# Optimization experiments

Hardware: AMD Instinct MI355X
Metric: run time of the kernel (lower is better)

Reference implementation:

```python
import jax, jax.numpy as jnp
import numpy as np

CHANNELS = 128


def setup_inputs() -> dict:
    key = jax.random.key(0)
    ks = jax.random.split(key, 7)
    B, N, C, E = 1, 50000, CHANNELS, 800000
    in_dim = 2 * C + 2  # channels*2 + 2
    tokens = jax.random.normal(ks[0], (B, N, C), dtype=jnp.float32)
    coords = jax.random.normal(ks[1], (B, N, 2), dtype=jnp.float32)
    edge_index = jax.random.randint(ks[2], (2, E), 0, N, dtype=jnp.int64)
    # MLP params: Linear(in_dim, C) -> ReLU -> Linear(C, 1)
    w1 = jax.random.normal(ks[3], (in_dim, C), dtype=jnp.float32) / np.sqrt(in_dim)
    b1 = jnp.zeros((C,), dtype=jnp.float32)
    w2 = jax.random.normal(ks[4], (C, 1), dtype=jnp.float32) / np.sqrt(C)
    b2 = jnp.zeros((1,), dtype=jnp.float32)
    return {"tokens": tokens, "coords": coords, "edge_index": edge_index,
            "w1": w1, "b1": b1, "w2": w2, "b2": b2}


def reference(tokens, coords, edge_index, w1, b1, w2, b2):
    src = edge_index[0]
    dst = edge_index[1]
    x_src = tokens[:, src, :]               # [B, E, C]
    x_dst = tokens[:, dst, :]               # [B, E, C]
    delta = coords[:, dst, :] - coords[:, src, :]  # [B, E, 2]
    feat = jnp.concatenate([x_src, x_dst, delta], axis=-1)  # [B, E, 2C+2]
    h = jax.nn.relu(jnp.einsum('bef,fh->beh', feat, w1) + b1)  # [B, E, C]
    return jnp.einsum('beh,ho->beo', h, w2) + b2               # [B, E, 1]
```

## Files before the change

kernel.cpp:

```cpp
#include <hip/hip_runtime.h>

static constexpr int CH   = 128;
static constexpr int KPAD = 192;

typedef __attribute__((ext_vector_type(8))) short bf16x8;
typedef __attribute__((ext_vector_type(4))) float f32x4;
typedef __attribute__((ext_vector_type(2))) unsigned int u32x2;

__device__ inline unsigned short f2bf(float x) {
    unsigned int u = __float_as_uint(x);
    unsigned int r = (u + 0x7fffu + ((u >> 16) & 1u)) >> 16;
    return (unsigned short)r;
}
__device__ inline unsigned int pack2bf(float a, float b) {
    return (unsigned int)f2bf(a) | ((unsigned int)f2bf(b) << 16);
}

__global__ __launch_bounds__(256) void idx_prep(
    const unsigned int* __restrict__ idxw, uint2* __restrict__ idx2,
    long long E, long long Epad) {
    unsigned nz = 0;
    const int lane = threadIdx.x & 63;
    for (int i = lane; i < 128; i += 64) nz |= idxw[2 * i + 1];
    const int is64 = (__ballot(nz != 0u) == 0ULL) ? 1 : 0;
    const long long stride = (long long)gridDim.x * blockDim.x;
    for (long long i = (long long)blockIdx.x * blockDim.x + threadIdx.x;
         i < Epad; i += stride) {
        uint2 v = make_uint2(0u, 0u);
        if (i < E) {
            const unsigned s = is64 ? idxw[2 * i] : idxw[i];
            const unsigned d = is64 ? idxw[2 * (E + i)] : idxw[E + i];
            v = make_uint2(s << 7, d << 7);
        }
        idx2[i] = v;
    }
}

__global__ __launch_bounds__(256) void w1_prep2(const float* __restrict__ w1,
                                                const float* __restrict__ b1,
                                                unsigned short* __restrict__ Wf) {
    const int gid = blockIdx.x * 256 + threadIdx.x;
    if (gid >= 4 * 5 * 4 * 64) return;
    const int lane = gid & 63;
    const int seg  = gid >> 6;
    const int m    = seg & 3;
    const int ks   = (seg >> 2) % 5;
    const int w    = seg / 20;
    const int c    = w * 64 + m * 16 + (lane & 15);
    const int k0   = ks * 32 + (lane >> 4) * 8;
    const bool isQ = c >= 128;
    const int cc   = c & 127;
    const float sgn = isQ ? 1.f : -1.f;
    unsigned int out[4];
#pragma unroll
    for (int h = 0; h < 4; ++h) {
        float v[2];
#pragma unroll
        for (int j = 0; j < 2; ++j) {
            const int k = k0 + 2 * h + j;
            float x;
            if (k < 128)       x = isQ ? w1[(size_t)(128 + k) * CH + cc]
                                       : w1[(size_t)k * CH + cc];
            else if (k == 128) x = sgn * w1[(size_t)(2 * CH) * CH + cc];
            else if (k == 129) x = sgn * w1[(size_t)(2 * CH + 1) * CH + cc];
            else if (k == 130) x = isQ ? b1[cc] : 0.f;
            else               x = 0.f;
            v[j] = x;
        }
        out[h] = pack2bf(v[0], v[1]);
    }
    *(uint4*)&Wf[(size_t)gid * 8] = make_uint4(out[0], out[1], out[2], out[3]);
}

__global__ __launch_bounds__(256) void node_mfma5(
    const float* __restrict__ tokens, const float* __restrict__ coords,
    const unsigned short* __restrict__ Wf, unsigned short* __restrict__ Plo,
    unsigned short* __restrict__ Phi, unsigned short* __restrict__ Qlo,
    unsigned short* __restrict__ Qhi, int N) {
    __shared__ unsigned short Atile[32 * KPAD];

    const int t    = threadIdx.x;
    const int l    = t & 63;
    const int wid  = t >> 6;
    const int n0   = blockIdx.x * 32;
    const int bl   = l & 15;
    const int bh   = l >> 4;

#pragma unroll
    for (int it = 0; it < 2; ++it) {
        const int idx  = it * 256 + t;
        const int node = idx >> 4;
        const int cq   = idx & 15;
        float4 v0 = make_float4(0.f, 0.f, 0.f, 0.f);
        float4 v1 = v0;
        if (n0 + node < N) {
            const float* src = &tokens[(size_t)(n0 + node) * CH + cq * 8];
            v0 = *(const float4*)src;
            v1 = *(const float4*)(src + 4);
        }
        uint4 u;
        u.x = pack2bf(v0.x, v0.y);
        u.y = pack2bf(v0.z, v0.w);
        u.z = pack2bf(v1.x, v1.y);
        u.w = pack2bf(v1.z, v1.w);
        const int byte = node * 384 + ((cq * 16) ^ ((node & 7) << 4));
        *(uint4*)((char*)Atile + byte) = u;
    }
    {
        const int node = t >> 3;
        const int ce   = t & 7;
        uint4 u = make_uint4(0u, 0u, 0u, 0u);
        if (ce == 0 && n0 + node < N) {
            const float cx = coords[2 * (n0 + node)];
            const float cy = coords[2 * (n0 + node) + 1];
            u.x = pack2bf(cx, cy);
            u.y = pack2bf(1.f, 0.f);
        }
        const int byte = node * 384 + (((16 + ce) * 16) ^ ((node & 7) << 4));
        *(uint4*)((char*)Atile + byte) = u;
    }
    __syncthreads();

    f32x4 acc[4][2];
#pragma unroll
    for (int m = 0; m < 4; ++m)
#pragma unroll
        for (int n = 0; n < 2; ++n) acc[m][n] = (f32x4){0.f, 0.f, 0.f, 0.f};

#pragma unroll
    for (int ks = 0; ks < 5; ++ks) {
        bf16x8 wfrag[4], tfrag[2];
#pragma unroll
        for (int m = 0; m < 4; ++m)
            wfrag[m] = *(const bf16x8*)&Wf[(size_t)(((wid * 5 + ks) * 4 + m) * 64
                                                    + l) * 8];
#pragma unroll
        for (int n = 0; n < 2; ++n) {
            const int row  = n * 16 + bl;
            const int byte = row * 384 + ((ks * 64 + bh * 16) ^ ((row & 7) << 4));
            tfrag[n] = *(const bf16x8*)((const char*)Atile + byte);
        }
#pragma unroll
        for (int m = 0; m < 4; ++m)
#pragma unroll
            for (int n = 0; n < 2; ++n)
                acc[m][n] = __builtin_amdgcn_mfma_f32_16x16x32_bf16(
                    wfrag[m], tfrag[n], acc[m][n], 0, 0, 0);
    }

    unsigned short* dst = (wid == 0) ? Plo : (wid == 1) ? Phi
                          : (wid == 2) ? Qlo : Qhi;
#pragma unroll
    for (int m = 0; m < 4; ++m) {
        const int col = m * 16 + bh * 4;
#pragma unroll
        for (int n = 0; n < 2; ++n) {
            const int node = n0 + n * 16 + bl;
            if (node < N) {
                uint2 val;
                val.x = pack2bf(acc[m][n][0], acc[m][n][1]);
                val.y = pack2bf(acc[m][n][2], acc[m][n][3]);
                *(uint2*)&dst[(size_t)node * 64 + col] = val;
            }
        }
    }
}

template <int PASS>
__global__ __launch_bounds__(256) void edge_pass(
    const unsigned int* __restrict__ idx2w, const unsigned short* __restrict__ Pb,
    const unsigned short* __restrict__ Qb, const float* __restrict__ w2,
    const float* __restrict__ b2, float* __restrict__ partial,
    float* __restrict__ out, long long E) {
    const int t  = threadIdx.x;
    const int gl = t & 7;
    const long long nq = (E + 3) >> 2;
    const long long g0 = (long long)blockIdx.x * 32 + (t >> 3);
    const long long ng = (long long)gridDim.x * 32;
    const float4 wa = *(const float4*)&w2[PASS * 64 + gl * 8];
    const float4 wb = *(const float4*)&w2[PASS * 64 + gl * 8 + 4];
    const float bias = b2[0];
    const char* P = (const char*)Pb;
    const char* Q = (const char*)Qb;

    for (long long q = g0; q < nq; q += ng) {
        const long long e0 = q << 2;
        const u32x2 iv = __builtin_nontemporal_load(
            (const u32x2*)&idx2w[(e0 + (gl & 3)) * 2]);
        unsigned soff[4], doff[4];
#pragma unroll
        for (int j = 0; j < 4; ++j) {
            soff[j] = __shfl(iv.x, j, 8);
            doff[j] = __shfl(iv.y, j, 8);
        }
        uint4 pv[4], qv[4];
#pragma unroll
        for (int j = 0; j < 4; ++j)
            pv[j] = *(const uint4*)(P + soff[j] + 16 * gl);
#pragma unroll
        for (int j = 0; j < 4; ++j)
            qv[j] = *(const uint4*)(Q + doff[j] + 16 * gl);

        float part[4];
#pragma unroll
        for (int j = 0; j < 4; ++j) {
            const float wv[8] = {wa.x, wa.y, wa.z, wa.w, wb.x, wb.y, wb.z, wb.w};
            const unsigned pw[4] = {pv[j].x, pv[j].y, pv[j].z, pv[j].w};
            const unsigned qw[4] = {qv[j].x, qv[j].y, qv[j].z, qv[j].w};
            float acc = 0.f;
#pragma unroll
            for (int i = 0; i < 4; ++i) {
                const float plo = __uint_as_float(pw[i] << 16);
                const float phi = __uint_as_float(pw[i] & 0xffff0000u);
                const float qlo = __uint_as_float(qw[i] << 16);
                const float qhi = __uint_as_float(qw[i] & 0xffff0000u);
                acc = fmaf(fmaxf(plo + qlo, 0.f), wv[2 * i], acc);
                acc = fmaf(fmaxf(phi + qhi, 0.f), wv[2 * i + 1], acc);
            }
            part[j] = acc;
        }

        float t0 = part[0] + __shfl_xor(part[0], 1);
        float t1 = part[1] + __shfl_xor(part[1], 1);
        float t2 = part[2] + __shfl_xor(part[2], 1);
        float t3 = part[3] + __shfl_xor(part[3], 1);
        float a0 = (gl & 1) ? t1 : t0;
        float a1 = (gl & 1) ? t3 : t2;
        a0 += __shfl_xor(a0, 2);
        a1 += __shfl_xor(a1, 2);
        float c = (gl & 2) ? a1 : a0;
        c += __shfl_xor(c, 4);

        const long long e = e0 + gl;
        if (gl < 4 && e < E) {
            if (PASS == 0) {
                __builtin_nontemporal_store(c, &partial[e]);
            } else {
                out[e] = __builtin_nontemporal_load(&partial[e]) + c + bias;
            }
        }
    }
}

extern "C" void kernel_launch(void* const* d_in, const int* in_sizes, int n_in,
                              void* d_out, int out_size, void* d_ws,
                              size_t ws_size, hipStream_t stream) {
    const float* tokens = (const float*)d_in[0];
    const float* coords = (const float*)d_in[1];
    const unsigned int* idxw = (const unsigned int*)d_in[2];
    const float* w1 = (const float*)d_in[3];
    const float* b1 = (const float*)d_in[4];
    const float* w2 = (const float*)d_in[5];
    const float* b2 = (const float*)d_in[6];
    float* out = (float*)d_out;

    const int N = in_sizes[0] / CH;
    const long long E = in_sizes[2] / 2;
    const long long Epad = ((E + 3) >> 2) << 2;

    unsigned short* Plo = (unsigned short*)d_ws;
    unsigned short* Phi = Plo + (size_t)N * 64;
    unsigned short* Qlo = Phi + (size_t)N * 64;
    unsigned short* Qhi = Qlo + (size_t)N * 64;
    uint2* idx2 = (uint2*)(Qhi + (size_t)N * 64);
    unsigned short* Wf = (unsigned short*)(idx2 + Epad);
    float* partial = (float*)(Wf + 5120 * 8);

    idx_prep<<<1024, 256, 0, stream>>>(idxw, idx2, E, Epad);
    w1_prep2<<<20, 256, 0, stream>>>(w1, b1, Wf);

    node_mfma5<<<(N + 31) / 32, 256, 0, stream>>>(tokens, coords, Wf,
                                                  Plo, Phi, Qlo, Qhi, N);

    edge_pass<0><<<4096, 256, 0, stream>>>((const unsigned int*)idx2, Plo, Qlo,
                                           w2, b2, partial, out, E);
    edge_pass<1><<<4096, 256, 0, stream>>>((const unsigned int*)idx2, Phi, Qhi,
                                           w2, b2, partial, out, E);
}
```

Baseline: 77.45 us.

## Split edge gather into four 32-channel passes with quarter-width node tables

Node projection outputs are stored as eight 32-channel bf16 slabs instead of four 64-channel slabs, and the edge stage runs as four passes, each gathering a 64-byte row per endpoint. The aim is to shrink each pass's gathered working set so the random row gathers fit better in cache. The cost is two extra kernel launches, more index reads, and extra read-modify-write traffic on the partial buffer.

```diff
diff --git a/kernel.cpp b/kernel.cpp
--- a/kernel.cpp
+++ b/kernel.cpp
@@ -30,7 +30,7 @@
         if (i < E) {
             const unsigned s = is64 ? idxw[2 * i] : idxw[i];
             const unsigned d = is64 ? idxw[2 * (E + i)] : idxw[E + i];
-            v = make_uint2(s << 7, d << 7);
+            v = make_uint2(s << 6, d << 6);
         }
         idx2[i] = v;
     }
@@ -72,11 +72,10 @@
     *(uint4*)&Wf[(size_t)gid * 8] = make_uint4(out[0], out[1], out[2], out[3]);
 }
 
-__global__ __launch_bounds__(256) void node_mfma5(
+__global__ __launch_bounds__(256) void node_mfma6(
     const float* __restrict__ tokens, const float* __restrict__ coords,
-    const unsigned short* __restrict__ Wf, unsigned short* __restrict__ Plo,
-    unsigned short* __restrict__ Phi, unsigned short* __restrict__ Qlo,
-    unsigned short* __restrict__ Qhi, int N) {
+    const unsigned short* __restrict__ Wf, unsigned short* __restrict__ PQall,
+    int N) {
     __shared__ unsigned short Atile[32 * KPAD];
 
     const int t    = threadIdx.x;
@@ -148,11 +147,12 @@
                     wfrag[m], tfrag[n], acc[m][n], 0, 0, 0);
     }
 
-    unsigned short* dst = (wid == 0) ? Plo : (wid == 1) ? Phi
-                          : (wid == 2) ? Qlo : Qhi;
 #pragma unroll
     for (int m = 0; m < 4; ++m) {
-        const int col = m * 16 + bh * 4;
+        const int c = wid * 64 + m * 16 + bh * 4;
+        const int q = (c < CH) ? (c >> 5) : (4 + ((c & 127) >> 5));
+        unsigned short* dst = PQall + (size_t)q * N * 32;
+        const int col = c & 31;
 #pragma unroll
         for (int n = 0; n < 2; ++n) {
             const int node = n0 + n * 16 + bl;
@@ -160,38 +160,37 @@
                 uint2 val;
                 val.x = pack2bf(acc[m][n][0], acc[m][n][1]);
                 val.y = pack2bf(acc[m][n][2], acc[m][n][3]);
-                *(uint2*)&dst[(size_t)node * 64 + col] = val;
+                *(uint2*)&dst[(size_t)node * 32 + col] = val;
             }
         }
     }
 }
 
 template <int PASS>
-__global__ __launch_bounds__(256) void edge_pass(
-    const unsigned int* __restrict__ idx2w, const unsigned short* __restrict__ Pb,
-    const unsigned short* __restrict__ Qb, const float* __restrict__ w2,
-    const float* __restrict__ b2, float* __restrict__ partial,
-    float* __restrict__ out, long long E) {
+__global__ __launch_bounds__(256) void edge_pass4(
+    const unsigned int* __restrict__ idx2w, const unsigned short* __restrict__ PQall,
+    const float* __restrict__ w2, const float* __restrict__ b2,
+    float* __restrict__ partial, float* __restrict__ out, long long E, int N) {
     const int t  = threadIdx.x;
-    const int gl = t & 7;
+    const int gl = t & 3;
     const long long nq = (E + 3) >> 2;
-    const long long g0 = (long long)blockIdx.x * 32 + (t >> 3);
-    const long long ng = (long long)gridDim.x * 32;
-    const float4 wa = *(const float4*)&w2[PASS * 64 + gl * 8];
-    const float4 wb = *(const float4*)&w2[PASS * 64 + gl * 8 + 4];
+    const long long g0 = (long long)blockIdx.x * 64 + (t >> 2);
+    const long long ng = (long long)gridDim.x * 64;
+    const float4 wa = *(const float4*)&w2[PASS * 32 + gl * 8];
+    const float4 wb = *(const float4*)&w2[PASS * 32 + gl * 8 + 4];
     const float bias = b2[0];
-    const char* P = (const char*)Pb;
-    const char* Q = (const char*)Qb;
+    const char* P = (const char*)(PQall + (size_t)PASS * N * 32);
+    const char* Q = (const char*)(PQall + (size_t)(4 + PASS) * N * 32);
 
     for (long long q = g0; q < nq; q += ng) {
         const long long e0 = q << 2;
         const u32x2 iv = __builtin_nontemporal_load(
-            (const u32x2*)&idx2w[(e0 + (gl & 3)) * 2]);
+            (const u32x2*)&idx2w[(e0 + gl) * 2]);
         unsigned soff[4], doff[4];
 #pragma unroll
         for (int j = 0; j < 4; ++j) {
-            soff[j] = __shfl(iv.x, j, 8);
-            doff[j] = __shfl(iv.y, j, 8);
+            soff[j] = __shfl(iv.x, j, 4);
+            doff[j] = __shfl(iv.y, j, 4);
         }
         uint4 pv[4], qv[4];
 #pragma unroll
@@ -228,13 +227,15 @@
         float a1 = (gl & 1) ? t3 : t2;
         a0 += __shfl_xor(a0, 2);
         a1 += __shfl_xor(a1, 2);
-        float c = (gl & 2) ? a1 : a0;
-        c += __shfl_xor(c, 4);
+        const float c = (gl & 2) ? a1 : a0;
 
         const long long e = e0 + gl;
-        if (gl < 4 && e < E) {
+        if (e < E) {
             if (PASS == 0) {
                 __builtin_nontemporal_store(c, &partial[e]);
+            } else if (PASS < 3) {
+                const float prev = __builtin_nontemporal_load(&partial[e]);
+                __builtin_nontemporal_store(prev + c, &partial[e]);
             } else {
                 out[e] = __builtin_nontemporal_load(&partial[e]) + c + bias;
             }
@@ -258,22 +259,19 @@
     const long long E = in_sizes[2] / 2;
     const long long Epad = ((E + 3) >> 2) << 2;
 
-    unsigned short* Plo = (unsigned short*)d_ws;
-    unsigned short* Phi = Plo + (size_t)N * 64;
-    unsigned short* Qlo = Phi + (size_t)N * 64;
-    unsigned short* Qhi = Qlo + (size_t)N * 64;
-    uint2* idx2 = (uint2*)(Qhi + (size_t)N * 64);
+    unsigned short* PQall = (unsigned short*)d_ws;
+    uint2* idx2 = (uint2*)(PQall + (size_t)N * CH * 2);
     unsigned short* Wf = (unsigned short*)(idx2 + Epad);
     float* partial = (float*)(Wf + 5120 * 8);
 
     idx_prep<<<1024, 256, 0, stream>>>(idxw, idx2, E, Epad);
     w1_prep2<<<20, 256, 0, stream>>>(w1, b1, Wf);
 
-    node_mfma5<<<(N + 31) / 32, 256, 0, stream>>>(tokens, coords, Wf,
-                                                  Plo, Phi, Qlo, Qhi, N);
-
-    edge_pass<0><<<4096, 256, 0, stream>>>((const unsigned int*)idx2, Plo, Qlo,
-                                           w2, b2, partial, out, E);
-    edge_pass<1><<<4096, 256, 0, stream>>>((const unsigned int*)idx2, Phi, Qhi,
-                                           w2, b2, partial, out, E);
-}
+    node_mfma6<<<(N + 31) / 32, 256, 0, stream>>>(tokens, coords, Wf, PQall, N);
+
+    const unsigned int* idx2w = (const unsigned int*)idx2;
+    edge_pass4<0><<<4096, 256, 0, stream>>>(idx2w, PQall, w2, b2, partial, out, E, N);
+    edge_pass4<1><<<4096, 256, 0, stream>>>(idx2w, PQall, w2, b2, partial, out, E, N);
+    edge_pass4<2><<<4096, 256, 0, stream>>>(idx2w, PQall, w2, b2, partial, out, E, N);
+    edge_pass4<3><<<4096, 256, 0, stream>>>(idx2w, PQall, w2, b2, partial, out, E, N);
+}
```

After: 95.43 us. 23.2% more time.
